# Optimization experiments

Hardware: AMD Instinct MI355X
Metric: run time of the kernel (lower is better)

## Reference

```python
import jax, jax.numpy as jnp
import numpy as np

BETA = 0.5
ITERS = 20


def bjorck_orthonormalize(w, beta, iters):
    def body(w, _):
        wtw = jnp.matmul(w.T, w)            # [in, in]
        w = (1.0 + beta) * w - beta * jnp.matmul(w, wtw)
        return w, None
    w, _ = jax.lax.scan(body, w, None, length=iters)
    return w


def setup_inputs() -> dict:
    key = jax.random.key(0)
    k1, k2, k3 = jax.random.split(key, 3)
    x = jax.random.normal(k1, (4, 8192, 1024), dtype=jnp.float32)
    kernel = jax.random.normal(k2, (1024, 1024), dtype=jnp.float32)
    bias = jax.random.normal(k3, (1024,), dtype=jnp.float32)
    return {"x": x, "kernel": kernel, "bias": bias}


def reference(x, kernel, bias):
    # safe Bjorck scaling: sqrt(in_features * out_features)
    scaling = jnp.sqrt(jnp.asarray(kernel.shape[0] * kernel.shape[1], dtype=kernel.dtype))
    w = bjorck_orthonormalize(kernel / scaling, BETA, ITERS)  # [in, out]
    y = jnp.einsum('bsi,io->bso', x, w)
    y = y + bias.reshape((1, 1, -1))
    return y
```

## Files before the change

kernel.cpp:

```cpp
#include <hip/hip_runtime.h>
#include <cstdint>

typedef _Float16 half8 __attribute__((ext_vector_type(8)));
typedef _Float16 half4v __attribute__((ext_vector_type(4)));
typedef float f32x4 __attribute__((ext_vector_type(4)));

__device__ __forceinline__ void async_copy16(const void* g, void* l) {
    __builtin_amdgcn_global_load_lds((const __attribute__((address_space(1))) void*)g,
                                     (__attribute__((address_space(3))) void*)l, 16, 0, 0);
}

__global__ __launch_bounds__(256) void prep_w(const float* __restrict__ K,
                                              _Float16* __restrict__ w0,
                                              _Float16* __restrict__ w0T) {
    __shared__ float tile[64][65];
    const int t  = threadIdx.x;
    const int bi = blockIdx.y * 64;
    const int bj = blockIdx.x * 64;
    const int r0 = t >> 4;
    const int c4 = (t & 15) * 4;
#pragma unroll
    for (int rr = 0; rr < 4; ++rr) {
        int r = r0 + rr * 16;
        f32x4 v = *(const f32x4*)&K[(size_t)(bi + r) * 1024 + bj + c4];
        v *= 0.03125f;
        half4v h;
        h[0] = (_Float16)v[0]; h[1] = (_Float16)v[1];
        h[2] = (_Float16)v[2]; h[3] = (_Float16)v[3];
        *(half4v*)&w0[(size_t)(bi + r) * 1024 + bj + c4] = h;
        tile[r][c4 + 0] = v[0]; tile[r][c4 + 1] = v[1];
        tile[r][c4 + 2] = v[2]; tile[r][c4 + 3] = v[3];
    }
    __syncthreads();
    const int cT = t >> 4;
    const int rT = (t & 15) * 4;
#pragma unroll
    for (int cc = 0; cc < 4; ++cc) {
        int c = cT + cc * 16;
        half4v h;
        h[0] = (_Float16)tile[rT + 0][c]; h[1] = (_Float16)tile[rT + 1][c];
        h[2] = (_Float16)tile[rT + 2][c]; h[3] = (_Float16)tile[rT + 3][c];
        *(half4v*)&w0T[(size_t)(bj + c) * 1024 + bi + rT] = h;
    }
}

template <int EPI>
__global__ __launch_bounds__(256) void gemm1k(const _Float16* __restrict__ A,
                                              const _Float16* __restrict__ BT,
                                              const _Float16* __restrict__ wcur,
                                              _Float16* __restrict__ out,
                                              _Float16* __restrict__ outT) {
    __shared__ _Float16 sA[2][64 * 64];
    __shared__ _Float16 sB[2][64 * 64];
    const int t   = threadIdx.x;
    const int m0  = blockIdx.y * 64, n0 = blockIdx.x * 64;
    const int ln  = t & 63, wv = t >> 6;
    const int wm  = wv >> 1, wn = wv & 1;
    const int q   = ln >> 4, l15 = ln & 15;

    f32x4 acc[2][2];
#pragma unroll
    for (int i = 0; i < 2; ++i)
#pragma unroll
        for (int j = 0; j < 2; ++j) {
            acc[i][j][0] = 0.f; acc[i][j][1] = 0.f;
            acc[i][j][2] = 0.f; acc[i][j][3] = 0.f;
        }

    auto stage = [&](int buf, int k0) {
#pragma unroll
        for (int rnd = 0; rnd < 2; ++rnd) {
            int c = t + rnd * 256;
            int row = c >> 3, s = c & 7;
            int gs = s ^ (row & 7);
            async_copy16(A + (size_t)(m0 + row) * 1024 + k0 + gs * 8, &sA[buf][c * 8]);
            async_copy16(BT + (size_t)(n0 + row) * 1024 + k0 + gs * 8, &sB[buf][c * 8]);
        }
    };

    auto frag = [&](const _Float16* s, int row, int kc) -> half8 {
        return *(const half8*)&s[row * 64 + ((kc ^ (row & 7)) << 3)];
    };

    stage(0, 0);
    int cur = 0;
#pragma unroll 1
    for (int it = 0; it < 16; ++it) {
        __syncthreads();
        if (it < 15) stage(cur ^ 1, (it + 1) * 64);
#pragma unroll
        for (int kk = 0; kk < 2; ++kk) {
            half8 a0 = frag(sA[cur], wm * 32 + 0  + l15, kk * 4 + q);
            half8 a1 = frag(sA[cur], wm * 32 + 16 + l15, kk * 4 + q);
            half8 b0 = frag(sB[cur], wn * 32 + 0  + l15, kk * 4 + q);
            half8 b1 = frag(sB[cur], wn * 32 + 16 + l15, kk * 4 + q);
            acc[0][0] = __builtin_amdgcn_mfma_f32_16x16x32_f16(a0, b0, acc[0][0], 0, 0, 0);
            acc[0][1] = __builtin_amdgcn_mfma_f32_16x16x32_f16(a0, b1, acc[0][1], 0, 0, 0);
            acc[1][0] = __builtin_amdgcn_mfma_f32_16x16x32_f16(a1, b0, acc[1][0], 0, 0, 0);
            acc[1][1] = __builtin_amdgcn_mfma_f32_16x16x32_f16(a1, b1, acc[1][1], 0, 0, 0);
        }
        cur ^= 1;
    }

#pragma unroll
    for (int im = 0; im < 2; ++im)
#pragma unroll
        for (int jn = 0; jn < 2; ++jn) {
            int row0 = m0 + wm * 32 + im * 16 + q * 4;
            int col  = n0 + wn * 32 + jn * 16 + l15;
            if (EPI == 0) {
#pragma unroll
                for (int r = 0; r < 4; ++r)
                    out[(size_t)(row0 + r) * 1024 + col] = (_Float16)acc[im][jn][r];
            } else {
                half4v hT;
#pragma unroll
                for (int r = 0; r < 4; ++r) {
                    float w0v = (float)wcur[(size_t)(row0 + r) * 1024 + col];
                    float nv  = 1.5f * w0v - 4.8828125e-4f * acc[im][jn][r];
                    _Float16 h = (_Float16)nv;
                    out[(size_t)(row0 + r) * 1024 + col] = h;
                    hT[r] = h;
                }
                *(half4v*)&outT[(size_t)col * 1024 + row0] = hT;
            }
        }
}

__global__ __launch_bounds__(256) void gemm_big(const float* __restrict__ X,
                                                const _Float16* __restrict__ BT,
                                                const float* __restrict__ bias,
                                                float* __restrict__ Y) {
    __shared__ _Float16 sA[2][128 * 40];
    __shared__ _Float16 sB[2][128 * 32];
    const int t  = threadIdx.x;
    const int m0 = blockIdx.y * 128, n0 = blockIdx.x * 128;
    const int ln = t & 63, wv = t >> 6;
    const int wm = wv >> 1, wn = wv & 1;
    const int q  = ln >> 4, l15 = ln & 15;

    f32x4 acc[4][4];
#pragma unroll
    for (int i = 0; i < 4; ++i)
#pragma unroll
        for (int j = 0; j < 4; ++j) {
            acc[i][j][0] = 0.f; acc[i][j][1] = 0.f;
            acc[i][j][2] = 0.f; acc[i][j][3] = 0.f;
        }

    auto loadA = [&](int k0, f32x4* va) {
#pragma unroll
        for (int rnd = 0; rnd < 4; ++rnd) {
            int c = t + rnd * 256;
            int row = c >> 3, s4 = c & 7;
            va[rnd] = *(const f32x4*)&X[(size_t)(m0 + row) * 1024 + k0 + s4 * 4];
        }
    };
    auto writeA = [&](int buf, const f32x4* va) {
#pragma unroll
        for (int rnd = 0; rnd < 4; ++rnd) {
            int c = t + rnd * 256;
            int row = c >> 3, s4 = c & 7;
            half4v h;
            h[0] = (_Float16)va[rnd][0]; h[1] = (_Float16)va[rnd][1];
            h[2] = (_Float16)va[rnd][2]; h[3] = (_Float16)va[rnd][3];
            *(half4v*)&sA[buf][row * 40 + s4 * 4] = h;
        }
    };
    auto stageB = [&](int buf, int k0) {
#pragma unroll
        for (int rnd = 0; rnd < 2; ++rnd) {
            int c = t + rnd * 256;
            int row = c >> 2, s = c & 3;
            int gs = s ^ ((row >> 1) & 3);
            async_copy16(BT + (size_t)(n0 + row) * 1024 + k0 + gs * 8, &sB[buf][c * 8]);
        }
    };

    f32x4 va[4];
    loadA(0, va);
    stageB(0, 0);
    writeA(0, va);
    int cur = 0;
#pragma unroll 1
    for (int it = 0; it < 32; ++it) {
        __syncthreads();
        if (it < 31) {
            loadA((it + 1) * 32, va);
            stageB(cur ^ 1, (it + 1) * 32);
        }
        half8 a[4], b[4];
#pragma unroll
        for (int im = 0; im < 4; ++im) {
            int row = wm * 64 + im * 16 + l15;
            a[im] = *(const half8*)&sA[cur][row * 40 + q * 8];
        }
#pragma unroll
        for (int jn = 0; jn < 4; ++jn) {
            int row = wn * 64 + jn * 16 + l15;
            b[jn] = *(const half8*)&sB[cur][row * 32 + ((q ^ ((row >> 1) & 3)) << 3)];
        }
#pragma unroll
        for (int im = 0; im < 4; ++im)
#pragma unroll
            for (int jn = 0; jn < 4; ++jn)
                acc[im][jn] = __builtin_amdgcn_mfma_f32_16x16x32_f16(a[im], b[jn], acc[im][jn], 0, 0, 0);
        if (it < 31) writeA(cur ^ 1, va);
        cur ^= 1;
    }

#pragma unroll
    for (int jn = 0; jn < 4; ++jn) {
        int col = n0 + wn * 64 + jn * 16 + l15;
        float bv = bias[col];
#pragma unroll
        for (int im = 0; im < 4; ++im) {
            int row0 = m0 + wm * 64 + im * 16 + q * 4;
#pragma unroll
            for (int r = 0; r < 4; ++r)
                Y[(size_t)(row0 + r) * 1024 + col] = acc[im][jn][r] * 0.03125f + bv;
        }
    }
}

extern "C" void kernel_launch(void* const* d_in, const int* in_sizes, int n_in,
                              void* d_out, int out_size, void* d_ws, size_t ws_size,
                              hipStream_t stream) {
    (void)in_sizes; (void)n_in; (void)out_size; (void)ws_size;
    const float* x    = (const float*)d_in[0];
    const float* kern = (const float*)d_in[1];
    const float* bias = (const float*)d_in[2];
    float* y = (float*)d_out;

    char* ws = (char*)d_ws;
    const size_t SZ = (size_t)1024 * 1024 * sizeof(_Float16);
    _Float16* wh[2] = {(_Float16*)(ws + 0 * SZ), (_Float16*)(ws + 1 * SZ)};
    _Float16* wT[2] = {(_Float16*)(ws + 2 * SZ), (_Float16*)(ws + 3 * SZ)};
    _Float16* Sh    = (_Float16*)(ws + 4 * SZ);

    prep_w<<<dim3(16, 16), 256, 0, stream>>>(kern, wh[0], wT[0]);

    for (int it = 0; it < 20; ++it) {
        int c = it & 1, n = c ^ 1;
        gemm1k<0><<<dim3(16, 16), 256, 0, stream>>>(wT[c], wT[c], nullptr, Sh, nullptr);
        gemm1k<1><<<dim3(16, 16), 256, 0, stream>>>(wh[c], Sh, wh[c], wh[n], wT[n]);
    }
    gemm_big<<<dim3(8, 256), 256, 0, stream>>>(x, wT[0], bias, y);
}
```

Before: 837.1 us.

## Fuse Bjorck iterations into persistent kernel with grid barriers; pre-convert X to fp16

Replaces the 40 separate small GEMM launches of the Bjorck loop with one persistent 256-block kernel that synchronises through atomic grid barriers, removing launch gaps and tail effects between iterations. The 1k GEMM tile depth doubles to 128 with a 16-way swizzle. When workspace allows, X is converted to fp16 in a separate pass so the big GEMM can stage both operands with async LDS copies. This costs an extra full read and write of X. The grid barrier assumes all 256 blocks are co-resident, which risks deadlock if they are not.

After: 1.918 ms. 2.29x slower.

```diff
diff --git a/kernel.cpp b/kernel.cpp
--- a/kernel.cpp
+++ b/kernel.cpp
@@ -10,11 +10,26 @@
                                      (__attribute__((address_space(3))) void*)l, 16, 0, 0);
 }
 
+__device__ __forceinline__ void grid_barrier(unsigned* bar, int slot) {
+    __syncthreads();
+    if (threadIdx.x == 0) {
+        __threadfence();
+        unsigned* p = bar + slot;
+        __hip_atomic_fetch_add(p, 1u, __ATOMIC_RELEASE, __HIP_MEMORY_SCOPE_AGENT);
+        while (__hip_atomic_load(p, __ATOMIC_ACQUIRE, __HIP_MEMORY_SCOPE_AGENT) < 256u)
+            __builtin_amdgcn_s_sleep(2);
+        __threadfence();
+    }
+    __syncthreads();
+}
+
 __global__ __launch_bounds__(256) void prep_w(const float* __restrict__ K,
                                               _Float16* __restrict__ w0,
-                                              _Float16* __restrict__ w0T) {
+                                              _Float16* __restrict__ w0T,
+                                              unsigned* __restrict__ bar) {
     __shared__ float tile[64][65];
     const int t  = threadIdx.x;
+    if (blockIdx.x == 0 && blockIdx.y == 0 && t < 64) bar[t] = 0u;
     const int bi = blockIdx.y * 64;
     const int bj = blockIdx.x * 64;
     const int r0 = t >> 4;
@@ -45,15 +60,13 @@
 }
 
 template <int EPI>
-__global__ __launch_bounds__(256) void gemm1k(const _Float16* __restrict__ A,
-                                              const _Float16* __restrict__ BT,
-                                              const _Float16* __restrict__ wcur,
-                                              _Float16* __restrict__ out,
-                                              _Float16* __restrict__ outT) {
-    __shared__ _Float16 sA[2][64 * 64];
-    __shared__ _Float16 sB[2][64 * 64];
-    const int t   = threadIdx.x;
-    const int m0  = blockIdx.y * 64, n0 = blockIdx.x * 64;
+__device__ __forceinline__ void gemm_phase(const _Float16* __restrict__ A,
+                                           const _Float16* __restrict__ BT,
+                                           const _Float16* __restrict__ wcur,
+                                           _Float16* __restrict__ out,
+                                           _Float16* __restrict__ outT,
+                                           _Float16 (*sA)[8192], _Float16 (*sB)[8192],
+                                           int m0, int n0, int t) {
     const int ln  = t & 63, wv = t >> 6;
     const int wm  = wv >> 1, wn = wv & 1;
     const int q   = ln >> 4, l15 = ln & 15;
@@ -69,27 +82,26 @@
 
     auto stage = [&](int buf, int k0) {
 #pragma unroll
-        for (int rnd = 0; rnd < 2; ++rnd) {
-            int c = t + rnd * 256;
-            int row = c >> 3, s = c & 7;
-            int gs = s ^ (row & 7);
+        for (int rnd = 0; rnd < 4; ++rnd) {
+            int c = t + rnd * 256;
+            int row = c >> 4, g = c & 15;
+            int gs = g ^ (row & 15);
             async_copy16(A + (size_t)(m0 + row) * 1024 + k0 + gs * 8, &sA[buf][c * 8]);
             async_copy16(BT + (size_t)(n0 + row) * 1024 + k0 + gs * 8, &sB[buf][c * 8]);
         }
     };
-
     auto frag = [&](const _Float16* s, int row, int kc) -> half8 {
-        return *(const half8*)&s[row * 64 + ((kc ^ (row & 7)) << 3)];
+        return *(const half8*)&s[row * 128 + ((kc ^ (row & 15)) << 3)];
     };
 
     stage(0, 0);
     int cur = 0;
 #pragma unroll 1
-    for (int it = 0; it < 16; ++it) {
+    for (int it = 0; it < 8; ++it) {
         __syncthreads();
-        if (it < 15) stage(cur ^ 1, (it + 1) * 64);
-#pragma unroll
-        for (int kk = 0; kk < 2; ++kk) {
+        if (it < 7) stage(cur ^ 1, (it + 1) * 128);
+#pragma unroll
+        for (int kk = 0; kk < 4; ++kk) {
             half8 a0 = frag(sA[cur], wm * 32 + 0  + l15, kk * 4 + q);
             half8 a1 = frag(sA[cur], wm * 32 + 16 + l15, kk * 4 + q);
             half8 b0 = frag(sB[cur], wn * 32 + 0  + l15, kk * 4 + q);
@@ -125,6 +137,114 @@
                 *(half4v*)&outT[(size_t)col * 1024 + row0] = hT;
             }
         }
+}
+
+__global__ __launch_bounds__(256) void bjorck_iter(_Float16* __restrict__ wh0,
+                                                   _Float16* __restrict__ wh1,
+                                                   _Float16* __restrict__ wT0,
+                                                   _Float16* __restrict__ wT1,
+                                                   _Float16* __restrict__ Sh,
+                                                   unsigned* __restrict__ bar) {
+    __shared__ _Float16 sA[2][8192];
+    __shared__ _Float16 sB[2][8192];
+    const int t  = threadIdx.x;
+    const int m0 = (blockIdx.x >> 4) * 64;
+    const int n0 = (blockIdx.x & 15) * 64;
+    _Float16* whp[2] = {wh0, wh1};
+    _Float16* wTp[2] = {wT0, wT1};
+
+#pragma unroll 1
+    for (int it = 0; it < 20; ++it) {
+        int c = it & 1, n = c ^ 1;
+        gemm_phase<0>(wTp[c], wTp[c], nullptr, Sh, nullptr, sA, sB, m0, n0, t);
+        grid_barrier(bar, 2 * it);
+        gemm_phase<1>(whp[c], Sh, whp[c], whp[n], wTp[n], sA, sB, m0, n0, t);
+        if (it < 19) grid_barrier(bar, 2 * it + 1);
+    }
+}
+
+__global__ __launch_bounds__(256) void xcvt(const float* __restrict__ X,
+                                            _Float16* __restrict__ Xh) {
+    size_t i = ((size_t)blockIdx.x * 256 + threadIdx.x) * 8;
+    f32x4 v0 = *(const f32x4*)&X[i];
+    f32x4 v1 = *(const f32x4*)&X[i + 4];
+    half8 h;
+    h[0] = (_Float16)v0[0]; h[1] = (_Float16)v0[1];
+    h[2] = (_Float16)v0[2]; h[3] = (_Float16)v0[3];
+    h[4] = (_Float16)v1[0]; h[5] = (_Float16)v1[1];
+    h[6] = (_Float16)v1[2]; h[7] = (_Float16)v1[3];
+    *(half8*)&Xh[i] = h;
+}
+
+__global__ __launch_bounds__(256) void gemm_big2(const _Float16* __restrict__ Xh,
+                                                 const _Float16* __restrict__ BT,
+                                                 const float* __restrict__ bias,
+                                                 float* __restrict__ Y) {
+    __shared__ _Float16 sA[2][4096];
+    __shared__ _Float16 sB[2][4096];
+    const int t  = threadIdx.x;
+    const int m0 = blockIdx.y * 128, n0 = blockIdx.x * 128;
+    const int ln = t & 63, wv = t >> 6;
+    const int wm = wv >> 1, wn = wv & 1;
+    const int q  = ln >> 4, l15 = ln & 15;
+
+    f32x4 acc[4][4];
+#pragma unroll
+    for (int i = 0; i < 4; ++i)
+#pragma unroll
+        for (int j = 0; j < 4; ++j) {
+            acc[i][j][0] = 0.f; acc[i][j][1] = 0.f;
+            acc[i][j][2] = 0.f; acc[i][j][3] = 0.f;
+        }
+
+    auto stage = [&](int buf, int k0) {
+#pragma unroll
+        for (int rnd = 0; rnd < 2; ++rnd) {
+            int c = t + rnd * 256;
+            int row = c >> 2, g = c & 3;
+            int gs = g ^ (row & 3);
+            async_copy16(Xh + (size_t)(m0 + row) * 1024 + k0 + gs * 8, &sA[buf][c * 8]);
+            async_copy16(BT + (size_t)(n0 + row) * 1024 + k0 + gs * 8, &sB[buf][c * 8]);
+        }
+    };
+
+    stage(0, 0);
+    int cur = 0;
+#pragma unroll 1
+    for (int it = 0; it < 32; ++it) {
+        __syncthreads();
+        if (it < 31) stage(cur ^ 1, (it + 1) * 32);
+        half8 a[4], b[4];
+#pragma unroll
+        for (int im = 0; im < 4; ++im) {
+            int row = wm * 64 + im * 16 + l15;
+            a[im] = *(const half8*)&sA[cur][row * 32 + ((q ^ (row & 3)) << 3)];
+        }
+#pragma unroll
+        for (int jn = 0; jn < 4; ++jn) {
+            int row = wn * 64 + jn * 16 + l15;
+            b[jn] = *(const half8*)&sB[cur][row * 32 + ((q ^ (row & 3)) << 3)];
+        }
+#pragma unroll
+        for (int im = 0; im < 4; ++im)
+#pragma unroll
+            for (int jn = 0; jn < 4; ++jn)
+                acc[im][jn] = __builtin_amdgcn_mfma_f32_16x16x32_f16(a[im], b[jn], acc[im][jn], 0, 0, 0);
+        cur ^= 1;
+    }
+
+#pragma unroll
+    for (int jn = 0; jn < 4; ++jn) {
+        int col = n0 + wn * 64 + jn * 16 + l15;
+        float bv = bias[col];
+#pragma unroll
+        for (int im = 0; im < 4; ++im) {
+            int row0 = m0 + wm * 64 + im * 16 + q * 4;
+#pragma unroll
+            for (int r = 0; r < 4; ++r)
+                Y[(size_t)(row0 + r) * 1024 + col] = acc[im][jn][r] * 0.03125f + bv;
+        }
+    }
 }
 
 __global__ __launch_bounds__(256) void gemm_big(const float* __restrict__ X,
@@ -226,7 +346,7 @@
 extern "C" void kernel_launch(void* const* d_in, const int* in_sizes, int n_in,
                               void* d_out, int out_size, void* d_ws, size_t ws_size,
                               hipStream_t stream) {
-    (void)in_sizes; (void)n_in; (void)out_size; (void)ws_size;
+    (void)in_sizes; (void)n_in; (void)out_size;
     const float* x    = (const float*)d_in[0];
     const float* kern = (const float*)d_in[1];
     const float* bias = (const float*)d_in[2];
@@ -237,13 +357,17 @@
     _Float16* wh[2] = {(_Float16*)(ws + 0 * SZ), (_Float16*)(ws + 1 * SZ)};
     _Float16* wT[2] = {(_Float16*)(ws + 2 * SZ), (_Float16*)(ws + 3 * SZ)};
     _Float16* Sh    = (_Float16*)(ws + 4 * SZ);
-
-    prep_w<<<dim3(16, 16), 256, 0, stream>>>(kern, wh[0], wT[0]);
-
-    for (int it = 0; it < 20; ++it) {
-        int c = it & 1, n = c ^ 1;
-        gemm1k<0><<<dim3(16, 16), 256, 0, stream>>>(wT[c], wT[c], nullptr, Sh, nullptr);
-        gemm1k<1><<<dim3(16, 16), 256, 0, stream>>>(wh[c], Sh, wh[c], wh[n], wT[n]);
-    }
-    gemm_big<<<dim3(8, 256), 256, 0, stream>>>(x, wT[0], bias, y);
-}
+    unsigned* bar   = (unsigned*)(ws + 5 * SZ);
+    _Float16* Xh    = (_Float16*)(ws + 5 * SZ + 4096);
+    const size_t XH_BYTES = (size_t)32768 * 1024 * 2;
+    const bool have_xh = ws_size >= 5 * SZ + 4096 + XH_BYTES;
+
+    prep_w<<<dim3(16, 16), 256, 0, stream>>>(kern, wh[0], wT[0], bar);
+    bjorck_iter<<<256, 256, 0, stream>>>(wh[0], wh[1], wT[0], wT[1], Sh, bar);
+    if (have_xh) {
+        xcvt<<<16384, 256, 0, stream>>>(x, Xh);
+        gemm_big2<<<dim3(8, 256), 256, 0, stream>>>(Xh, wT[0], bias, y);
+    } else {
+        gemm_big<<<dim3(8, 256), 256, 0, stream>>>(x, wT[0], bias, y);
+    }
+}
```
